# Kernel tuning notes

Hardware: AMD Instinct MI355X
Metric: run time of the kernel (lower is better)

## Reference

```python
import jax, jax.numpy as jnp
import numpy as np

DIM = 4096
N_HEADS = 32
HEAD_DIM = 128
N_KV = 8
REP = N_HEADS // N_KV  # 4
B = 8       # number of packed sequences (block-diagonal blocks)
S = 1024    # tokens per sequence
T = B * S   # seqlen_sum = 8192


def setup_inputs() -> dict:
    key = jax.random.key(0)
    ks = jax.random.split(key, 6)
    x = jax.random.normal(ks[0], (T, DIM), dtype=jnp.float32)
    # RoPE freqs: positions restart at 0 for each packed sequence
    pos = jnp.tile(jnp.arange(S, dtype=jnp.float32), B)            # [T]
    inv_freq = 1.0 / (10000.0 ** (jnp.arange(0, HEAD_DIM, 2, dtype=jnp.float32) / HEAD_DIM))  # [HEAD_DIM//2]
    freqs = pos[:, None] * inv_freq[None, :]                       # [T, HEAD_DIM//2]
    cos = jnp.cos(freqs)
    sin = jnp.sin(freqs)
    s = 0.02
    wq = jax.random.normal(ks[1], (DIM, N_HEADS * HEAD_DIM), dtype=jnp.float32) * s
    wk = jax.random.normal(ks[2], (DIM, N_KV * HEAD_DIM), dtype=jnp.float32) * s
    wv = jax.random.normal(ks[3], (DIM, N_KV * HEAD_DIM), dtype=jnp.float32) * s
    wo = jax.random.normal(ks[4], (N_HEADS * HEAD_DIM, DIM), dtype=jnp.float32) * s
    return {"x": x, "cos": cos, "sin": sin, "wq": wq, "wk": wk, "wv": wv, "wo": wo}


def _rope(t, cos, sin):
    # t: [T, H, D]; cos/sin: [T, D//2]; complex rotation on (even, odd) pairs
    th, hd = t.shape[1], t.shape[2]
    tp = t.reshape(t.shape[0], th, hd // 2, 2)
    te, to = tp[..., 0], tp[..., 1]
    c = cos[:, None, :]
    s = sin[:, None, :]
    oe = te * c - to * s
    oo = te * s + to * c
    return jnp.stack([oe, oo], axis=-1).reshape(t.shape)


def reference(x, cos, sin, wq, wk, wv, wo):
    scale = HEAD_DIM ** -0.5
    q = (x @ wq).reshape(T, N_HEADS, HEAD_DIM)
    k = (x @ wk).reshape(T, N_KV, HEAD_DIM)
    v = (x @ wv).reshape(T, N_KV, HEAD_DIM)
    q = _rope(q, cos, sin)
    k = _rope(k, cos, sin)
    # Block-diagonal mask with equal blocks == batched attention over B sequences.
    # GQA: q head index h = kv*REP + r (matches repeat_interleave on kv dim),
    # so group q heads as [N_KV, REP] instead of materializing repeated K/V.
    q = q.reshape(B, S, N_KV, REP, HEAD_DIM)
    k = k.reshape(B, S, N_KV, HEAD_DIM)
    v = v.reshape(B, S, N_KV, HEAD_DIM)
    scores = jnp.einsum('bqkrd,bskd->bkrqs', q, k) * scale   # [B, N_KV, REP, S, S]
    attn = jax.nn.softmax(scores, axis=-1)
    out = jnp.einsum('bkrqs,bskd->bqkrd', attn, v)           # [B, S, N_KV, REP, D]
    out = out.reshape(T, N_HEADS * HEAD_DIM)
    return out @ wo
```

## Files before the change

### kernel.cpp

```cpp
#include <hip/hip_runtime.h>
#include <math.h>

typedef unsigned short ushort_t;
typedef __attribute__((ext_vector_type(8))) short short8;
typedef __attribute__((ext_vector_type(4))) float f32x4;

#define MFMA16(a, b, c) __builtin_amdgcn_mfma_f32_16x16x32_bf16(a, b, c, 0, 0, 0)

__device__ __forceinline__ ushort_t f2bf(float f) {
    union { float f; unsigned u; } v;
    v.f = f;
    unsigned r = v.u + 0x7FFF + ((v.u >> 16) & 1);
    return (ushort_t)(r >> 16);
}

__device__ __forceinline__ void gload_lds16(const ushort_t* g, ushort_t* l) {
    __builtin_amdgcn_global_load_lds(
        (const __attribute__((address_space(1))) void*)g,
        (__attribute__((address_space(3))) void*)l, 16, 0, 0);
}

__global__ __launch_bounds__(256) void cast_f32_bf16(const float* __restrict__ src,
                                                     ushort_t* __restrict__ dst, int n8) {
    int i = blockIdx.x * 256 + threadIdx.x;
    if (i >= n8) return;
    const float4* s = (const float4*)src;
    float4 a = s[2 * i], b = s[2 * i + 1];
    union { ushort_t u[8]; uint4 v; } o;
    o.u[0] = f2bf(a.x); o.u[1] = f2bf(a.y); o.u[2] = f2bf(a.z); o.u[3] = f2bf(a.w);
    o.u[4] = f2bf(b.x); o.u[5] = f2bf(b.y); o.u[6] = f2bf(b.z); o.u[7] = f2bf(b.w);
    ((uint4*)dst)[i] = o.v;
}

__global__ __launch_bounds__(256) void transpose_cast64(const float* __restrict__ src,
                                                        int D, int N,
                                                        ushort_t* __restrict__ dst, int dstStride) {
    __shared__ float t[64][33];
    int n0 = blockIdx.x * 32, d0 = blockIdx.y * 64;
    {
        int tx = threadIdx.x & 31, ty = threadIdx.x >> 5;
#pragma unroll
        for (int i = 0; i < 8; i++)
            t[ty + 8 * i][tx] = src[(size_t)(d0 + ty + 8 * i) * N + n0 + tx];
    }
    __syncthreads();
    {
        int tx = threadIdx.x & 63, ty = threadIdx.x >> 6;
#pragma unroll
        for (int i = 0; i < 8; i++) {
            int n = ty + 4 * i;
            dst[(size_t)(n0 + n) * dstStride + d0 + tx] = f2bf(t[tx][n]);
        }
    }
}

__global__ __launch_bounds__(256) void transpose_v(const ushort_t* __restrict__ qkv,
                                                   ushort_t* __restrict__ vt) {
    __shared__ ushort_t t[32][33];
    int bk = blockIdx.z; int b = bk >> 3, kvh = bk & 7;
    int s0 = blockIdx.x * 32, d0 = blockIdx.y * 32;
    int tx = threadIdx.x & 31, ty = threadIdx.x >> 5;
#pragma unroll
    for (int i = 0; i < 4; i++)
        t[ty + 8 * i][tx] = qkv[(size_t)(b * 1024 + s0 + ty + 8 * i) * 6144 + 5120 + kvh * 128 + d0 + tx];
    __syncthreads();
#pragma unroll
    for (int i = 0; i < 4; i++)
        vt[((size_t)(b * 8 + kvh) * 128 + d0 + ty + 8 * i) * 1024 + s0 + tx] = t[tx][ty + 8 * i];
}

template <int EPI>
__global__ __launch_bounds__(512, 2) void gemm17(
    const ushort_t* __restrict__ A, const ushort_t* __restrict__ Bt,
    ushort_t* __restrict__ obf, float* __restrict__ of32,
    int M, int N, int K,
    const float* __restrict__ cosT, const float* __restrict__ sinT) {
    extern __shared__ __align__(16) ushort_t lds[];
    const int tid = threadIdx.x;
    const int lane = tid & 63, wv = tid >> 6;
    const int wr = wv >> 2, wc = wv & 3;
    const int lr = lane & 15, g = lane >> 4;

    const int gx = gridDim.x;
    const int nwg = gx * gridDim.y;
    const int bid = blockIdx.y * gx + blockIdx.x;
    const int swz = (bid & 7) * (nwg >> 3) + (bid >> 3);
    const int brow = (swz / gx) * 256, bcol = (swz % gx) * 256;

    const int st_r = tid >> 3, st_p = tid & 7;
    const int cA = (st_p ^ (st_r & 7)) * 8;
    const int dstT = st_r * 64 + st_p * 8;

    const ushort_t* sAq[4];
    const ushort_t* sBq[4];
#pragma unroll
    for (int q = 0; q < 4; ++q) {
        sAq[q] = A + (size_t)(brow + q * 64 + st_r) * K + cA;
        sBq[q] = Bt + (size_t)(bcol + q * 64 + st_r) * K + cA;
    }

    const int sl0 = (g ^ (lr & 7)) * 8;
    const int sl1 = ((4 + g) ^ (lr & 7)) * 8;
    const ushort_t* pA0 = lds + (wr * 128 + lr) * 64 + sl0;
    const ushort_t* pA1 = lds + (wr * 128 + lr) * 64 + sl1;
    const ushort_t* pB0 = lds + 49152 + (wc * 64 + lr) * 64 + sl0;
    const ushort_t* pB1 = lds + 49152 + (wc * 64 + lr) * 64 + sl1;

    f32x4 acc[8][4];
#pragma unroll
    for (int m = 0; m < 8; m++)
#pragma unroll
        for (int n = 0; n < 4; n++) acc[m][n] = (f32x4){0.f, 0.f, 0.f, 0.f};

#define STG_A(kn, q, SLOT) \
    gload_lds16(sAq[q] + (size_t)(kn) * 64, lds + (SLOT) * 16384 + (q) * 4096 + dstT)
#define STG_B(kn, q, SLOT) \
    gload_lds16(sBq[q] + (size_t)(kn) * 64, lds + 49152 + (SLOT) * 16384 + (q) * 4096 + dstT)

    STG_B(0, 0, 0); STG_B(0, 1, 0); STG_B(0, 2, 0); STG_B(0, 3, 0);
    STG_A(0, 0, 0); STG_A(0, 1, 0); STG_A(0, 2, 0); STG_A(0, 3, 0);
    STG_A(1, 0, 1); STG_A(1, 1, 1); STG_A(1, 2, 1); STG_A(1, 3, 1);

#define TILE(SA, SB, kt, LAST)                                                       \
    {                                                                                \
        short8 bfr[4], af[4];                                                        \
                        \
        if (LAST) asm volatile("s_waitcnt vmcnt(0)" ::: "memory");                   \
        else      asm volatile("s_waitcnt vmcnt(4)" ::: "memory");                   \
        __builtin_amdgcn_s_barrier();                                                \
        __builtin_amdgcn_sched_barrier(0);                                           \
        _Pragma("unroll")                                                            \
        for (int n = 0; n < 4; ++n)                                                  \
            bfr[n] = *(const short8*)(pB0 + (SB) * 16384 + n * 1024);                \
        _Pragma("unroll")                                                            \
        for (int m = 0; m < 4; ++m)                                                  \
            af[m] = *(const short8*)(pA0 + (SA) * 16384 + m * 1024);                 \
        if ((kt) + 1 < 64) { STG_B((kt) + 1, 0, (SB) ^ 1); STG_B((kt) + 1, 1, (SB) ^ 1); } \
        __builtin_amdgcn_s_setprio(1);                                               \
        _Pragma("unroll")                                                            \
        for (int m = 0; m < 4; ++m)                                                  \
            _Pragma("unroll")                                                        \
            for (int n = 0; n < 4; ++n) acc[m][n] = MFMA16(af[m], bfr[n], acc[m][n]); \
        __builtin_amdgcn_s_setprio(0);                                               \
          \
        __builtin_amdgcn_s_barrier();                                                \
        __builtin_amdgcn_sched_barrier(0);                                           \
        _Pragma("unroll")                                                            \
        for (int m = 0; m < 4; ++m)                                                  \
            af[m] = *(const short8*)(pA0 + (SA) * 16384 + 4096 + m * 1024);          \
        if ((kt) + 1 < 64) { STG_B((kt) + 1, 2, (SB) ^ 1); STG_B((kt) + 1, 3, (SB) ^ 1); } \
        __builtin_amdgcn_s_setprio(1);                                               \
        _Pragma("unroll")                                                            \
        for (int m = 0; m < 4; ++m)                                                  \
            _Pragma("unroll")                                                        \
            for (int n = 0; n < 4; ++n) acc[m + 4][n] = MFMA16(af[m], bfr[n], acc[m + 4][n]); \
        __builtin_amdgcn_s_setprio(0);                                               \
                                                       \
        __builtin_amdgcn_s_barrier();                                                \
        __builtin_amdgcn_sched_barrier(0);                                           \
        _Pragma("unroll")                                                            \
        for (int n = 0; n < 4; ++n)                                                  \
            bfr[n] = *(const short8*)(pB1 + (SB) * 16384 + n * 1024);                \
        _Pragma("unroll")                                                            \
        for (int m = 0; m < 4; ++m)                                                  \
            af[m] = *(const short8*)(pA1 + (SA) * 16384 + m * 1024);                 \
        if ((kt) + 2 < 64) { STG_A((kt) + 2, 0, ((SA) + 2) % 3); STG_A((kt) + 2, 1, ((SA) + 2) % 3); } \
        __builtin_amdgcn_s_setprio(1);                                               \
        _Pragma("unroll")                                                            \
        for (int m = 0; m < 4; ++m)                                                  \
            _Pragma("unroll")                                                        \
            for (int n = 0; n < 4; ++n) acc[m][n] = MFMA16(af[m], bfr[n], acc[m][n]); \
        __builtin_amdgcn_s_setprio(0);                                               \
                                                       \
        __builtin_amdgcn_s_barrier();                                                \
        __builtin_amdgcn_sched_barrier(0);                                           \
        _Pragma("unroll")                                                            \
        for (int m = 0; m < 4; ++m)                                                  \
            af[m] = *(const short8*)(pA1 + (SA) * 16384 + 4096 + m * 1024);          \
        if ((kt) + 2 < 64) { STG_A((kt) + 2, 2, ((SA) + 2) % 3); STG_A((kt) + 2, 3, ((SA) + 2) % 3); } \
        __builtin_amdgcn_s_setprio(1);                                               \
        _Pragma("unroll")                                                            \
        for (int m = 0; m < 4; ++m)                                                  \
            _Pragma("unroll")                                                        \
            for (int n = 0; n < 4; ++n) acc[m + 4][n] = MFMA16(af[m], bfr[n], acc[m + 4][n]); \
        __builtin_amdgcn_s_setprio(0);                                               \
    }

    for (int kt0 = 0; kt0 < 60; kt0 += 6) {
        TILE(0, 0, kt0 + 0, false);
        TILE(1, 1, kt0 + 1, false);
        TILE(2, 0, kt0 + 2, false);
        TILE(0, 1, kt0 + 3, false);
        TILE(1, 0, kt0 + 4, false);
        TILE(2, 1, kt0 + 5, false);
    }
    TILE(0, 0, 60, false);
    TILE(1, 1, 61, false);
    TILE(2, 0, 62, false);
    TILE(0, 1, 63, true);
#undef TILE
#undef STG_A
#undef STG_B

#pragma unroll
    for (int m = 0; m < 8; ++m) {
#pragma unroll
        for (int n = 0; n < 4; ++n) {
#pragma unroll
            for (int reg = 0; reg < 4; ++reg) {
                int r = brow + wr * 128 + m * 16 + g * 4 + reg;
                int c = bcol + wc * 64 + n * 16 + lr;
                float val = acc[m][n][reg];
                if (EPI == 1) {
                    float other = __shfl_xor(val, 1, 64);
                    if (c < 5120) {
                        int pos = r & 1023;
                        int pair = (c & 127) >> 1;
                        float cz = cosT[pos * 64 + pair];
                        float sz = sinT[pos * 64 + pair];
                        val = val * cz + other * ((c & 1) ? sz : -sz);
                        if (c < 4096) val *= 0.12752551286084110f;
                    }
                    obf[(size_t)r * N + c] = f2bf(val);
                } else {
                    of32[(size_t)r * N + c] = val;
                }
            }
        }
    }
}

__global__ __launch_bounds__(512, 2) void attn_fwd2(const ushort_t* __restrict__ qkv,
                                                    const ushort_t* __restrict__ vt,
                                                    ushort_t* __restrict__ aout) {
    extern __shared__ __align__(16) ushort_t lds[];
    const int tid = threadIdx.x, lane = tid & 63, w = tid >> 6;
    const int lr = lane & 15, g = lane >> 4;
    const int hr = w & 3, qc = w >> 2;
    const int qt = blockIdx.x, kvh = blockIdx.y, b = blockIdx.z;
    const int h = kvh * 4 + hr;
    const size_t qRow0 = (size_t)b * 1024 + qt * 64 + qc * 32;
    const size_t kBase = (size_t)b * 1024 * 6144 + 4096 + kvh * 128;
    const size_t vBase = (size_t)(b * 8 + kvh) * 128 * 1024;
    ushort_t* Pw = lds + 32768 + w * 2304;

    short8 qf[2][4];
#pragma unroll
    for (int qg = 0; qg < 2; ++qg)
#pragma unroll
        for (int kd = 0; kd < 4; ++kd)
            qf[qg][kd] = *(const short8*)&qkv[(qRow0 + qg * 16 + lr) * 6144 + h * 128 + kd * 32 + g * 8];

    f32x4 o[2][8];
#pragma unroll
    for (int qg = 0; qg < 2; ++qg)
#pragma unroll
        for (int nd = 0; nd < 8; ++nd) o[qg][nd] = (f32x4){0.f, 0.f, 0.f, 0.f};
    f32x4 lsum[2];
    lsum[0] = (f32x4){0.f, 0.f, 0.f, 0.f};
    lsum[1] = (f32x4){0.f, 0.f, 0.f, 0.f};

#define STAGE_KV(kt)                                                                   \
    {                                                                                  \
        const int buf_ = (kt) & 1;                                                     \
        {                                                                              \
            const int r0_ = tid >> 4, p_ = tid & 15;                                   \
            gload_lds16(qkv + kBase + (size_t)((kt) * 64 + r0_) * 6144 + ((p_ ^ (r0_ & 7)) * 8), \
                        lds + buf_ * 8192 + r0_ * 128 + p_ * 8);                       \
            const int r1_ = r0_ + 32;                                                  \
            gload_lds16(qkv + kBase + (size_t)((kt) * 64 + r1_) * 6144 + ((p_ ^ (r1_ & 7)) * 8), \
                        lds + buf_ * 8192 + r1_ * 128 + p_ * 8);                       \
        }                                                                              \
        {                                                                              \
            const int d0_ = tid >> 3, p_ = tid & 7;                                    \
            gload_lds16(vt + vBase + (size_t)d0_ * 1024 + (kt) * 64 + ((p_ ^ (d0_ & 7)) * 8), \
                        lds + 16384 + buf_ * 8192 + d0_ * 64 + p_ * 8);                \
            const int d1_ = d0_ + 64;                                                  \
            gload_lds16(vt + vBase + (size_t)d1_ * 1024 + (kt) * 64 + ((p_ ^ (d1_ & 7)) * 8), \
                        lds + 16384 + buf_ * 8192 + d1_ * 64 + p_ * 8);                \
        }                                                                              \
    }

    STAGE_KV(0);

    for (int kt = 0; kt < 16; ++kt) {
        const int buf = kt & 1;
        if (kt < 15) {
            STAGE_KV(kt + 1);
            asm volatile("s_waitcnt vmcnt(4)" ::: "memory");
        } else {
            asm volatile("s_waitcnt vmcnt(0)" ::: "memory");
        }
        __builtin_amdgcn_s_barrier();

        f32x4 sc[2][4];
#pragma unroll
        for (int qg = 0; qg < 2; ++qg)
#pragma unroll
            for (int ns = 0; ns < 4; ++ns) sc[qg][ns] = (f32x4){0.f, 0.f, 0.f, 0.f};
        __builtin_amdgcn_s_setprio(1);
#pragma unroll
        for (int ns = 0; ns < 4; ++ns) {
            const int key = ns * 16 + lr;
#pragma unroll
            for (int kd = 0; kd < 4; ++kd) {
                const short8 kf = *(const short8*)(lds + buf * 8192 + key * 128 +
                                                   (((kd * 4 + g) ^ (lr & 7)) * 8));
                sc[0][ns] = MFMA16(qf[0][kd], kf, sc[0][ns]);
                sc[1][ns] = MFMA16(qf[1][kd], kf, sc[1][ns]);
            }
        }
        __builtin_amdgcn_s_setprio(0);

#pragma unroll
        for (int qg = 0; qg < 2; ++qg) {
#pragma unroll
            for (int ns = 0; ns < 4; ++ns) {
#pragma unroll
                for (int j = 0; j < 4; ++j) {
                    float p = exp2f(sc[qg][ns][j]);
                    sc[qg][ns][j] = p;
                    lsum[qg][j] += p;
                }
            }
        }
#pragma unroll
        for (int qg = 0; qg < 2; ++qg)
#pragma unroll
            for (int ns = 0; ns < 4; ++ns)
#pragma unroll
                for (int j = 0; j < 4; ++j)
                    Pw[(qg * 16 + g * 4 + j) * 72 + ns * 16 + lr] = f2bf(sc[qg][ns][j]);

        __builtin_amdgcn_s_setprio(1);
#pragma unroll
        for (int ks = 0; ks < 2; ++ks) {
            short8 pa[2];
            pa[0] = *(const short8*)(Pw + (0 + lr) * 72 + ks * 32 + g * 8);
            pa[1] = *(const short8*)(Pw + (16 + lr) * 72 + ks * 32 + g * 8);
#pragma unroll
            for (int nd = 0; nd < 8; ++nd) {
                const int d = nd * 16 + lr;
                const short8 vf = *(const short8*)(lds + 16384 + buf * 8192 + d * 64 +
                                                   (((ks * 4 + g) ^ (d & 7)) * 8));
                o[0][nd] = MFMA16(pa[0], vf, o[0][nd]);
                o[1][nd] = MFMA16(pa[1], vf, o[1][nd]);
            }
        }
        __builtin_amdgcn_s_setprio(0);
        __builtin_amdgcn_s_barrier();
    }
#undef STAGE_KV

#pragma unroll
    for (int qg = 0; qg < 2; ++qg) {
#pragma unroll
        for (int j = 0; j < 4; ++j) {
            float s = lsum[qg][j];
            s += __shfl_xor(s, 1, 64);
            s += __shfl_xor(s, 2, 64);
            s += __shfl_xor(s, 4, 64);
            s += __shfl_xor(s, 8, 64);
            const float inv = 1.0f / s;
            const size_t r = qRow0 + qg * 16 + g * 4 + j;
#pragma unroll
            for (int nd = 0; nd < 8; ++nd)
                aout[r * 4096 + h * 128 + nd * 16 + lr] = f2bf(o[qg][nd][j] * inv);
        }
    }
}

extern "C" void kernel_launch(void* const* d_in, const int* in_sizes, int n_in,
                              void* d_out, int out_size, void* d_ws, size_t ws_size,
                              hipStream_t stream) {
    const float* x    = (const float*)d_in[0];
    const float* cosT = (const float*)d_in[1];
    const float* sinT = (const float*)d_in[2];
    const float* wq   = (const float*)d_in[3];
    const float* wk   = (const float*)d_in[4];
    const float* wv   = (const float*)d_in[5];
    const float* wo   = (const float*)d_in[6];
    float* out = (float*)d_out;

    char* ws = (char*)d_ws;
    ushort_t* xb   = (ushort_t*)(ws);
    ushort_t* wT   = (ushort_t*)(ws + 67108864);
    ushort_t* woT  = (ushort_t*)(ws + 117440512);
    ushort_t* qkv  = (ushort_t*)(ws + 150994944);
    ushort_t* vtb  = (ushort_t*)(ws + 67108864);
    ushort_t* attn = (ushort_t*)(ws);

    hipFuncSetAttribute((const void*)gemm17<1>, hipFuncAttributeMaxDynamicSharedMemorySize, 163840);
    hipFuncSetAttribute((const void*)gemm17<2>, hipFuncAttributeMaxDynamicSharedMemorySize, 163840);
    hipFuncSetAttribute((const void*)attn_fwd2, hipFuncAttributeMaxDynamicSharedMemorySize, 102400);

    cast_f32_bf16<<<16384, 256, 0, stream>>>(x, xb, 8192 * 4096 / 8);
    transpose_cast64<<<dim3(128, 64), 256, 0, stream>>>(wq, 4096, 4096, wT, 4096);
    transpose_cast64<<<dim3(32, 64), 256, 0, stream>>>(wk, 4096, 1024, wT + (size_t)4096 * 4096, 4096);
    transpose_cast64<<<dim3(32, 64), 256, 0, stream>>>(wv, 4096, 1024, wT + (size_t)5120 * 4096, 4096);
    transpose_cast64<<<dim3(128, 64), 256, 0, stream>>>(wo, 4096, 4096, woT, 4096);

    gemm17<1><<<dim3(24, 32), 512, 163840, stream>>>(xb, wT, qkv, nullptr, 8192, 6144, 4096, cosT, sinT);
    transpose_v<<<dim3(32, 4, 64), 256, 0, stream>>>(qkv, vtb);
    attn_fwd2<<<dim3(16, 8, 8), 512, 102400, stream>>>(qkv, vtb, attn);
    gemm17<2><<<dim3(16, 32), 512, 163840, stream>>>(attn, woT, nullptr, out, 8192, 4096, 4096, nullptr, nullptr);
}
```

Baseline: 911.1 us.

## Use 16 waves per GEMM block with 64-row warp tiles instead of 8 waves

The GEMM now launches 1024 threads (16 waves) per 256x256 block, so each wave covers a 64x64 output tile instead of 128x64. Accumulators and A fragments shrink by half, and each thread issues half as many global-to-LDS loads per stage, with the vmcnt wait adjusted to match. The goal is more resident waves to hide latency and lower per-wave register pressure. In exchange, LDS B-fragment reads are duplicated across more waves and barriers synchronize twice as many waves.

```diff
diff --git a/kernel.cpp b/kernel.cpp
--- a/kernel.cpp
+++ b/kernel.cpp
@@ -70,7 +70,7 @@
 }
 
 template <int EPI>
-__global__ __launch_bounds__(512, 2) void gemm17(
+__global__ __launch_bounds__(1024, 4) void gemm18(
     const ushort_t* __restrict__ A, const ushort_t* __restrict__ Bt,
     ushort_t* __restrict__ obf, float* __restrict__ of32,
     int M, int N, int K,
@@ -91,42 +91,42 @@
     const int cA = (st_p ^ (st_r & 7)) * 8;
     const int dstT = st_r * 64 + st_p * 8;
 
-    const ushort_t* sAq[4];
-    const ushort_t* sBq[4];
-#pragma unroll
-    for (int q = 0; q < 4; ++q) {
-        sAq[q] = A + (size_t)(brow + q * 64 + st_r) * K + cA;
-        sBq[q] = Bt + (size_t)(bcol + q * 64 + st_r) * K + cA;
+    const ushort_t* sAh[2];
+    const ushort_t* sBh[2];
+#pragma unroll
+    for (int h = 0; h < 2; ++h) {
+        sAh[h] = A + (size_t)(brow + h * 128 + st_r) * K + cA;
+        sBh[h] = Bt + (size_t)(bcol + h * 128 + st_r) * K + cA;
     }
 
     const int sl0 = (g ^ (lr & 7)) * 8;
     const int sl1 = ((4 + g) ^ (lr & 7)) * 8;
-    const ushort_t* pA0 = lds + (wr * 128 + lr) * 64 + sl0;
-    const ushort_t* pA1 = lds + (wr * 128 + lr) * 64 + sl1;
+    const ushort_t* pA0 = lds + (wr * 64 + lr) * 64 + sl0;
+    const ushort_t* pA1 = lds + (wr * 64 + lr) * 64 + sl1;
     const ushort_t* pB0 = lds + 49152 + (wc * 64 + lr) * 64 + sl0;
     const ushort_t* pB1 = lds + 49152 + (wc * 64 + lr) * 64 + sl1;
 
-    f32x4 acc[8][4];
-#pragma unroll
-    for (int m = 0; m < 8; m++)
+    f32x4 acc[4][4];
+#pragma unroll
+    for (int m = 0; m < 4; m++)
 #pragma unroll
         for (int n = 0; n < 4; n++) acc[m][n] = (f32x4){0.f, 0.f, 0.f, 0.f};
 
-#define STG_A(kn, q, SLOT) \
-    gload_lds16(sAq[q] + (size_t)(kn) * 64, lds + (SLOT) * 16384 + (q) * 4096 + dstT)
-#define STG_B(kn, q, SLOT) \
-    gload_lds16(sBq[q] + (size_t)(kn) * 64, lds + 49152 + (SLOT) * 16384 + (q) * 4096 + dstT)
-
-    STG_B(0, 0, 0); STG_B(0, 1, 0); STG_B(0, 2, 0); STG_B(0, 3, 0);
-    STG_A(0, 0, 0); STG_A(0, 1, 0); STG_A(0, 2, 0); STG_A(0, 3, 0);
-    STG_A(1, 0, 1); STG_A(1, 1, 1); STG_A(1, 2, 1); STG_A(1, 3, 1);
+#define STG_A(kn, h, SLOT) \
+    gload_lds16(sAh[h] + (size_t)(kn) * 64, lds + (SLOT) * 16384 + (h) * 8192 + dstT)
+#define STG_B(kn, h, SLOT) \
+    gload_lds16(sBh[h] + (size_t)(kn) * 64, lds + 49152 + (SLOT) * 16384 + (h) * 8192 + dstT)
+
+    STG_B(0, 0, 0); STG_B(0, 1, 0);
+    STG_A(0, 0, 0); STG_A(0, 1, 0);
+    STG_A(1, 0, 1); STG_A(1, 1, 1);
 
 #define TILE(SA, SB, kt, LAST)                                                       \
     {                                                                                \
         short8 bfr[4], af[4];                                                        \
-                        \
+                       \
         if (LAST) asm volatile("s_waitcnt vmcnt(0)" ::: "memory");                   \
-        else      asm volatile("s_waitcnt vmcnt(4)" ::: "memory");                   \
+        else      asm volatile("s_waitcnt vmcnt(2)" ::: "memory");                   \
         __builtin_amdgcn_s_barrier();                                                \
         __builtin_amdgcn_sched_barrier(0);                                           \
         _Pragma("unroll")                                                            \
@@ -142,20 +142,7 @@
             _Pragma("unroll")                                                        \
             for (int n = 0; n < 4; ++n) acc[m][n] = MFMA16(af[m], bfr[n], acc[m][n]); \
         __builtin_amdgcn_s_setprio(0);                                               \
-          \
-        __builtin_amdgcn_s_barrier();                                                \
-        __builtin_amdgcn_sched_barrier(0);                                           \
-        _Pragma("unroll")                                                            \
-        for (int m = 0; m < 4; ++m)                                                  \
-            af[m] = *(const short8*)(pA0 + (SA) * 16384 + 4096 + m * 1024);          \
-        if ((kt) + 1 < 64) { STG_B((kt) + 1, 2, (SB) ^ 1); STG_B((kt) + 1, 3, (SB) ^ 1); } \
-        __builtin_amdgcn_s_setprio(1);                                               \
-        _Pragma("unroll")                                                            \
-        for (int m = 0; m < 4; ++m)                                                  \
-            _Pragma("unroll")                                                        \
-            for (int n = 0; n < 4; ++n) acc[m + 4][n] = MFMA16(af[m], bfr[n], acc[m + 4][n]); \
-        __builtin_amdgcn_s_setprio(0);                                               \
-                                                       \
+                                                             \
         __builtin_amdgcn_s_barrier();                                                \
         __builtin_amdgcn_sched_barrier(0);                                           \
         _Pragma("unroll")                                                            \
@@ -170,19 +157,6 @@
         for (int m = 0; m < 4; ++m)                                                  \
             _Pragma("unroll")                                                        \
             for (int n = 0; n < 4; ++n) acc[m][n] = MFMA16(af[m], bfr[n], acc[m][n]); \
-        __builtin_amdgcn_s_setprio(0);                                               \
-                                                       \
-        __builtin_amdgcn_s_barrier();                                                \
-        __builtin_amdgcn_sched_barrier(0);                                           \
-        _Pragma("unroll")                                                            \
-        for (int m = 0; m < 4; ++m)                                                  \
-            af[m] = *(const short8*)(pA1 + (SA) * 16384 + 4096 + m * 1024);          \
-        if ((kt) + 2 < 64) { STG_A((kt) + 2, 2, ((SA) + 2) % 3); STG_A((kt) + 2, 3, ((SA) + 2) % 3); } \
-        __builtin_amdgcn_s_setprio(1);                                               \
-        _Pragma("unroll")                                                            \
-        for (int m = 0; m < 4; ++m)                                                  \
-            _Pragma("unroll")                                                        \
-            for (int n = 0; n < 4; ++n) acc[m + 4][n] = MFMA16(af[m], bfr[n], acc[m + 4][n]); \
         __builtin_amdgcn_s_setprio(0);                                               \
     }
 
@@ -203,12 +177,12 @@
 #undef STG_B
 
 #pragma unroll
-    for (int m = 0; m < 8; ++m) {
+    for (int m = 0; m < 4; ++m) {
 #pragma unroll
         for (int n = 0; n < 4; ++n) {
 #pragma unroll
             for (int reg = 0; reg < 4; ++reg) {
-                int r = brow + wr * 128 + m * 16 + g * 4 + reg;
+                int r = brow + wr * 64 + m * 16 + g * 4 + reg;
                 int c = bcol + wc * 64 + n * 16 + lr;
                 float val = acc[m][n][reg];
                 if (EPI == 1) {
@@ -390,8 +364,8 @@
     ushort_t* vtb  = (ushort_t*)(ws + 67108864);
     ushort_t* attn = (ushort_t*)(ws);
 
-    hipFuncSetAttribute((const void*)gemm17<1>, hipFuncAttributeMaxDynamicSharedMemorySize, 163840);
-    hipFuncSetAttribute((const void*)gemm17<2>, hipFuncAttributeMaxDynamicSharedMemorySize, 163840);
+    hipFuncSetAttribute((const void*)gemm18<1>, hipFuncAttributeMaxDynamicSharedMemorySize, 163840);
+    hipFuncSetAttribute((const void*)gemm18<2>, hipFuncAttributeMaxDynamicSharedMemorySize, 163840);
     hipFuncSetAttribute((const void*)attn_fwd2, hipFuncAttributeMaxDynamicSharedMemorySize, 102400);
 
     cast_f32_bf16<<<16384, 256, 0, stream>>>(x, xb, 8192 * 4096 / 8);
@@ -400,8 +374,8 @@
     transpose_cast64<<<dim3(32, 64), 256, 0, stream>>>(wv, 4096, 1024, wT + (size_t)5120 * 4096, 4096);
     transpose_cast64<<<dim3(128, 64), 256, 0, stream>>>(wo, 4096, 4096, woT, 4096);
 
-    gemm17<1><<<dim3(24, 32), 512, 163840, stream>>>(xb, wT, qkv, nullptr, 8192, 6144, 4096, cosT, sinT);
+    gemm18<1><<<dim3(24, 32), 1024, 163840, stream>>>(xb, wT, qkv, nullptr, 8192, 6144, 4096, cosT, sinT);
     transpose_v<<<dim3(32, 4, 64), 256, 0, stream>>>(qkv, vtb);
     attn_fwd2<<<dim3(16, 8, 8), 512, 102400, stream>>>(qkv, vtb, attn);
-    gemm17<2><<<dim3(16, 32), 512, 163840, stream>>>(attn, woT, nullptr, out, 8192, 4096, 4096, nullptr, nullptr);
-}
+    gemm18<2><<<dim3(16, 32), 1024, 163840, stream>>>(attn, woT, nullptr, out, 8192, 4096, 4096, nullptr, nullptr);
+}
```

After: 956.6 us. +5.0%, slower.
